# Kernel optimization log

Hardware: AMD Instinct MI355X
Metric: run time of the kernel (lower is better)

Reference implementation:

```python
import jax, jax.numpy as jnp
import numpy as np

N_NODES = 20000
N_EDGES = 200000
D_IN, D_H1, D_H2, D_OUT = 1433, 1000, 500, 7


def setup_inputs() -> dict:
    key = jax.random.key(0)
    ks = jax.random.split(key, 8)
    features = jax.random.normal(ks[0], (N_NODES, D_IN), dtype=jnp.float32)
    src = jax.random.randint(ks[1], (N_EDGES,), 0, N_NODES)
    dst = jax.random.randint(ks[2], (N_EDGES,), 0, N_NODES)
    W1 = jax.random.normal(ks[3], (D_IN, D_H1), dtype=jnp.float32) * 0.02
    b1 = jnp.zeros((D_H1,), dtype=jnp.float32)
    W2 = jax.random.normal(ks[4], (D_H1, D_H2), dtype=jnp.float32) * 0.02
    b2 = jnp.zeros((D_H2,), dtype=jnp.float32)
    W3 = jax.random.normal(ks[5], (D_H2, D_OUT), dtype=jnp.float32) * 0.02
    b3 = jnp.zeros((D_OUT,), dtype=jnp.float32)
    return {"features": features, "src": src, "dst": dst,
            "W1": W1, "b1": b1, "W2": W2, "b2": b2, "W3": W3, "b3": b3}


def reference(features, src, dst, W1, b1, W2, b2, W3, b3):
    N = features.shape[0]

    def agg(x):  # sum_tensors over incoming neighbors: h_i = sum_{(j->i) in E} x_j
        return jax.ops.segment_sum(x[src], dst, num_segments=N)

    # GCN layer 1: aggregate -> linear -> relu
    x = jax.nn.relu(agg(features) @ W1 + b1)       # [N, 1000]
    # GCN layer 2: aggregate -> linear -> relu (dropout = identity in eval)
    x = jax.nn.relu(agg(x) @ W2 + b2)              # [N, 500]
    # output linear -> relu (dropout = identity in eval)
    x = jax.nn.relu(x @ W3 + b3)                   # [N, 7]
    return x
```

## Files before the change

### kernel.cpp

```cpp
#include <hip/hip_runtime.h>
#include <hip/hip_bf16.h>


#define N_NODES 20000
#define N_EDGES 200000
#define D_IN    1433
#define D_H1    1000
#define D_H2    500
#define D_OUT   7

#define MPAD    20096
#define K1PAD   1472
#define N1PAD   1024
#define K2PAD   1024
#define N2PAD   512
#define MBLK    157
#define SCAN_N  (N_NODES + 1)
#define TB1     ((N1PAD / 32) * (K1PAD / 32))
#define TB2     ((N2PAD / 32) * (K2PAD / 32))
#define CNTB    ((N_EDGES + 255) / 256)

typedef __attribute__((ext_vector_type(8))) short short8;
typedef __attribute__((ext_vector_type(8))) unsigned short ushort8_t;
typedef __attribute__((ext_vector_type(4))) float f32x4;

__device__ __forceinline__ unsigned short bf16_rne(float x) {
    unsigned int u = __float_as_uint(x);
    u = (u + 0x7FFFu + ((u >> 16) & 1u)) >> 16;
    return (unsigned short)u;
}
__device__ __forceinline__ float bf16_up(unsigned short h) {
    return __uint_as_float((unsigned int)h << 16);
}

__device__ __forceinline__ void gl_lds16(const unsigned short* g, unsigned short* lds) {
    __builtin_amdgcn_global_load_lds(
        (const __attribute__((address_space(1))) unsigned int*)g,
        (__attribute__((address_space(3))) unsigned int*)lds, 16, 0, 0);
}

__global__ __launch_bounds__(256) void prep(const float* __restrict__ F,
                                            unsigned int* __restrict__ Fout,
                                            const float* __restrict__ W1,
                                            unsigned short* __restrict__ W1T,
                                            const float* __restrict__ W2,
                                            unsigned short* __restrict__ W2T,
                                            const int* __restrict__ dst,
                                            int* __restrict__ offs) {
    __shared__ float tile[32][33];
    const int bid = blockIdx.x, t = threadIdx.x;
    if (bid < MPAD) {
        int e = bid * 256 + t;
        if (e < N_EDGES) atomicAdd(&offs[dst[e] + 1], 1);
        const float* fr = F + (size_t)bid * D_IN;
        bool live = bid < N_NODES;
        for (int kk = t; kk < K1PAD / 2; kk += 256) {
            int k0 = kk * 2;
            float a = (live && k0     < D_IN) ? fr[k0]     : 0.f;
            float b = (live && k0 + 1 < D_IN) ? fr[k0 + 1] : 0.f;
            Fout[(size_t)bid * (K1PAD / 2) + kk] =
                (unsigned int)bf16_rne(a) | ((unsigned int)bf16_rne(b) << 16);
        }
        return;
    }
    const float* src; unsigned short* dstp;
    int SR, SC, DR, DC, bx, by;
    if (bid < MPAD + TB1) {
        int l = bid - MPAD;
        bx = l % (N1PAD / 32); by = l / (N1PAD / 32);
        src = W1; dstp = W1T; SR = D_IN; SC = D_H1; DR = N1PAD; DC = K1PAD;
    } else {
        int l = bid - MPAD - TB1;
        bx = l % (N2PAD / 32); by = l / (N2PAD / 32);
        src = W2; dstp = W2T; SR = D_H1; SC = D_H2; DR = N2PAD; DC = K2PAD;
    }
    const int c0 = bx * 32, r0 = by * 32;
    const int tx = t & 31, ty = t >> 5;
    #pragma unroll
    for (int p = 0; p < 4; ++p) {
        int r = r0 + ty + p * 8, c = c0 + tx;
        tile[ty + p * 8][tx] = (r < SR && c < SC) ? src[(size_t)r * SC + c] : 0.f;
    }
    __syncthreads();
    #pragma unroll
    for (int p = 0; p < 4; ++p) {
        int dr = c0 + ty + p * 8;
        int dc = r0 + tx;
        if (dr < DR && dc < DC) dstp[(size_t)dr * DC + dc] = bf16_rne(tile[tx][ty + p * 8]);
    }
}

__global__ __launch_bounds__(1024) void scan_csr(int* __restrict__ offs) {
    __shared__ int wsum[16];
    const int t = threadIdx.x, lane = t & 63, wv = t >> 6;
    const int base = t * 20;
    int v[20];
    int run = 0;
    #pragma unroll
    for (int k = 0; k < 20; ++k) {
        int i = base + k;
        int x = (i < SCAN_N) ? offs[i] : 0;
        run += x;
        v[k] = run;
    }
    const int tot = run;
    int w = tot;
    #pragma unroll
    for (int s = 1; s < 64; s <<= 1) {
        int u = __shfl_up(w, s, 64);
        if (lane >= s) w += u;
    }
    if (lane == 63) wsum[wv] = w;
    __syncthreads();
    int prefix = w - tot;
    for (int k = 0; k < wv; ++k) prefix += wsum[k];
    #pragma unroll
    for (int k = 0; k < 20; ++k) {
        int i = base + k;
        if (i < SCAN_N) offs[i] = prefix + v[k];
    }
}

__global__ __launch_bounds__(256) void fill_csr(const int* __restrict__ src,
                                                const int* __restrict__ dst,
                                                int* __restrict__ offs,
                                                int* __restrict__ srcs) {
    int e = blockIdx.x * 256 + threadIdx.x;
    if (e < N_EDGES) {
        int pos = atomicAdd(&offs[dst[e]], 1);
        srcs[pos] = src[e];
    }
}

template <int KPAD, int NB>
__global__ __launch_bounds__(256) void gemm_mfma(const unsigned short* __restrict__ A,
                                                 const unsigned short* __restrict__ B,
                                                 unsigned short* __restrict__ C,
                                                 int M, int OSTR) {
    __shared__ __align__(16) unsigned short sA[128 * 64];
    __shared__ __align__(16) unsigned short sB[128 * 64];
    const int bid = blockIdx.x;
    const int xcd = bid & 7;
    const int tt  = bid >> 3;
    const int nb  = tt % NB;
    const int mb  = (tt / NB) * 8 + xcd;
    if (mb >= MBLK) return;

    const int t = threadIdx.x;
    const int w = t >> 6, lane = t & 63;
    const int m0 = mb * 128, n0 = nb * 128;
    const int wm = (w >> 1) * 64, wn = (w & 1) * 64;

    const int srowo = lane >> 3;
    const int skc   = ((lane & 7) ^ srowo) * 8;
    const int mrow = lane & 15, quad = lane >> 4;

    const unsigned short* Aptr = A + (size_t)(m0 + srowo) * KPAD + skc;
    const unsigned short* Bptr = B + (size_t)(n0 + srowo) * KPAD + skc;

    f32x4 acc[4][4] = {};

    for (int k0 = 0; k0 < KPAD; k0 += 64) {
        #pragma unroll
        for (int c = 0; c < 4; ++c) {
            const int rbase = c * 32 + w * 8;
            gl_lds16(Aptr + (size_t)rbase * KPAD, &sA[rbase * 64]);
            gl_lds16(Bptr + (size_t)rbase * KPAD, &sB[rbase * 64]);
        }
        Aptr += 64; Bptr += 64;
        __syncthreads();

        #pragma unroll
        for (int s = 0; s < 2; ++s) {
            short8 af[4], bf[4];
            #pragma unroll
            for (int mt = 0; mt < 4; ++mt) {
                int r = wm + mt * 16 + mrow;
                af[mt] = *(const short8*)&sA[r * 64 + (((s * 4 + quad) ^ (mrow & 7)) * 8)];
            }
            #pragma unroll
            for (int nt = 0; nt < 4; ++nt) {
                int r = wn + nt * 16 + mrow;
                bf[nt] = *(const short8*)&sB[r * 64 + (((s * 4 + quad) ^ (mrow & 7)) * 8)];
            }
            #pragma unroll
            for (int mt = 0; mt < 4; ++mt)
                #pragma unroll
                for (int nt = 0; nt < 4; ++nt)
                    acc[mt][nt] = __builtin_amdgcn_mfma_f32_16x16x32_bf16(
                        af[mt], bf[nt], acc[mt][nt], 0, 0, 0);
        }
        __syncthreads();
    }

    #pragma unroll
    for (int mt = 0; mt < 4; ++mt) {
        int m = m0 + wm + mt * 16 + quad * 4;
        #pragma unroll
        for (int nt = 0; nt < 4; ++nt) {
            int n = n0 + wn + nt * 16 + mrow;
            if (n >= OSTR) continue;
            #pragma unroll
            for (int r = 0; r < 4; ++r)
                if (m + r < M) C[(size_t)(m + r) * OSTR + n] = bf16_rne(acc[mt][nt][r]);
        }
    }
}

__global__ __launch_bounds__(128) void agg1_bf16(const unsigned short* __restrict__ H,
                                                 const int* __restrict__ offs,
                                                 const int* __restrict__ srcs,
                                                 const float* __restrict__ bias,
                                                 unsigned short* __restrict__ X,
                                                 int hstr) {
    const int i = blockIdx.x, t = threadIdx.x;
    const bool active = t < 125;
    const int tc = active ? t : 124;
    ushort8_t o = (ushort8_t)0;
    if (i < N_NODES) {
        const int end = offs[i];
        const int beg = i ? offs[i - 1] : 0;
        const unsigned short* Hc = H + tc * 8;
        float s[8] = {};
        int e = beg;
        for (; e + 8 <= end; e += 8) {
            int j0 = srcs[e],     j1 = srcs[e + 1], j2 = srcs[e + 2], j3 = srcs[e + 3];
            int j4 = srcs[e + 4], j5 = srcs[e + 5], j6 = srcs[e + 6], j7 = srcs[e + 7];
            ushort8_t v0 = *(const ushort8_t*)(Hc + (size_t)j0 * hstr);
            ushort8_t v1 = *(const ushort8_t*)(Hc + (size_t)j1 * hstr);
            ushort8_t v2 = *(const ushort8_t*)(Hc + (size_t)j2 * hstr);
            ushort8_t v3 = *(const ushort8_t*)(Hc + (size_t)j3 * hstr);
            ushort8_t v4 = *(const ushort8_t*)(Hc + (size_t)j4 * hstr);
            ushort8_t v5 = *(const ushort8_t*)(Hc + (size_t)j5 * hstr);
            ushort8_t v6 = *(const ushort8_t*)(Hc + (size_t)j6 * hstr);
            ushort8_t v7 = *(const ushort8_t*)(Hc + (size_t)j7 * hstr);
            #pragma unroll
            for (int u = 0; u < 8; ++u) {
                float t0 = (bf16_up(v0[u]) + bf16_up(v1[u])) +
                           (bf16_up(v2[u]) + bf16_up(v3[u]));
                float t1 = (bf16_up(v4[u]) + bf16_up(v5[u])) +
                           (bf16_up(v6[u]) + bf16_up(v7[u]));
                s[u] += t0 + t1;
            }
        }
        for (; e + 4 <= end; e += 4) {
            int j0 = srcs[e], j1 = srcs[e + 1], j2 = srcs[e + 2], j3 = srcs[e + 3];
            ushort8_t v0 = *(const ushort8_t*)(Hc + (size_t)j0 * hstr);
            ushort8_t v1 = *(const ushort8_t*)(Hc + (size_t)j1 * hstr);
            ushort8_t v2 = *(const ushort8_t*)(Hc + (size_t)j2 * hstr);
            ushort8_t v3 = *(const ushort8_t*)(Hc + (size_t)j3 * hstr);
            #pragma unroll
            for (int u = 0; u < 8; ++u)
                s[u] += (bf16_up(v0[u]) + bf16_up(v1[u])) +
                        (bf16_up(v2[u]) + bf16_up(v3[u]));
        }
        for (; e < end; ++e) {
            ushort8_t v = *(const ushort8_t*)(Hc + (size_t)srcs[e] * hstr);
            #pragma unroll
            for (int u = 0; u < 8; ++u) s[u] += bf16_up(v[u]);
        }
        if (active) {
            #pragma unroll
            for (int u = 0; u < 8; ++u)
                o[u] = bf16_rne(fmaxf(s[u] + bias[t * 8 + u], 0.f));
        }
    }
    *(ushort8_t*)(X + (size_t)i * K2PAD + t * 8) = o;
}

__global__ __launch_bounds__(64) void agg2_out(const unsigned short* __restrict__ H,
                                               const int* __restrict__ offs,
                                               const int* __restrict__ srcs,
                                               const float* __restrict__ b2,
                                               const float* __restrict__ W3,
                                               const float* __restrict__ b3,
                                               float* __restrict__ out,
                                               int hstr) {
    const int i = blockIdx.x, t = threadIdx.x;
    const int tc = t < 63 ? t : 62;
    const int end = offs[i];
    const int beg = i ? offs[i - 1] : 0;
    const unsigned short* Hc = H + tc * 8;
    float s[8] = {};
    int e = beg;
    for (; e + 8 <= end; e += 8) {
        int j0 = srcs[e],     j1 = srcs[e + 1], j2 = srcs[e + 2], j3 = srcs[e + 3];
        int j4 = srcs[e + 4], j5 = srcs[e + 5], j6 = srcs[e + 6], j7 = srcs[e + 7];
        ushort8_t v0 = *(const ushort8_t*)(Hc + (size_t)j0 * hstr);
        ushort8_t v1 = *(const ushort8_t*)(Hc + (size_t)j1 * hstr);
        ushort8_t v2 = *(const ushort8_t*)(Hc + (size_t)j2 * hstr);
        ushort8_t v3 = *(const ushort8_t*)(Hc + (size_t)j3 * hstr);
        ushort8_t v4 = *(const ushort8_t*)(Hc + (size_t)j4 * hstr);
        ushort8_t v5 = *(const ushort8_t*)(Hc + (size_t)j5 * hstr);
        ushort8_t v6 = *(const ushort8_t*)(Hc + (size_t)j6 * hstr);
        ushort8_t v7 = *(const ushort8_t*)(Hc + (size_t)j7 * hstr);
        #pragma unroll
        for (int u = 0; u < 8; ++u) {
            float t0 = (bf16_up(v0[u]) + bf16_up(v1[u])) +
                       (bf16_up(v2[u]) + bf16_up(v3[u]));
            float t1 = (bf16_up(v4[u]) + bf16_up(v5[u])) +
                       (bf16_up(v6[u]) + bf16_up(v7[u]));
            s[u] += t0 + t1;
        }
    }
    for (; e + 4 <= end; e += 4) {
        int j0 = srcs[e], j1 = srcs[e + 1], j2 = srcs[e + 2], j3 = srcs[e + 3];
        ushort8_t v0 = *(const ushort8_t*)(Hc + (size_t)j0 * hstr);
        ushort8_t v1 = *(const ushort8_t*)(Hc + (size_t)j1 * hstr);
        ushort8_t v2 = *(const ushort8_t*)(Hc + (size_t)j2 * hstr);
        ushort8_t v3 = *(const ushort8_t*)(Hc + (size_t)j3 * hstr);
        #pragma unroll
        for (int u = 0; u < 8; ++u)
            s[u] += (bf16_up(v0[u]) + bf16_up(v1[u])) +
                    (bf16_up(v2[u]) + bf16_up(v3[u]));
    }
    for (; e < end; ++e) {
        ushort8_t v = *(const ushort8_t*)(Hc + (size_t)srcs[e] * hstr);
        #pragma unroll
        for (int u = 0; u < 8; ++u) s[u] += bf16_up(v[u]);
    }

    float acc[D_OUT] = {};
    if (t < 63) {
        #pragma unroll
        for (int u = 0; u < 8; ++u) {
            int col = t * 8 + u;
            if (col < D_H2) {
                float x = fmaxf(s[u] + b2[col], 0.f);
                const float* wr = W3 + (size_t)col * D_OUT;
                #pragma unroll
                for (int j = 0; j < D_OUT; ++j) acc[j] += x * wr[j];
            }
        }
    }
    #pragma unroll
    for (int j = 0; j < D_OUT; ++j)
        #pragma unroll
        for (int off = 32; off; off >>= 1) acc[j] += __shfl_down(acc[j], off);
    if (t == 0) {
        #pragma unroll
        for (int j = 0; j < D_OUT; ++j)
            out[(size_t)i * D_OUT + j] = fmaxf(acc[j] + b3[j], 0.f);
    }
}

extern "C" void kernel_launch(void* const* d_in, const int* in_sizes, int n_in,
                              void* d_out, int out_size, void* d_ws, size_t ws_size,
                              hipStream_t stream) {
    const float* features = (const float*)d_in[0];
    const int*   src      = (const int*)d_in[1];
    const int*   dst      = (const int*)d_in[2];
    const float* W1       = (const float*)d_in[3];
    const float* b1       = (const float*)d_in[4];
    const float* W2       = (const float*)d_in[5];
    const float* b2       = (const float*)d_in[6];
    const float* W3       = (const float*)d_in[7];
    const float* b3       = (const float*)d_in[8];
    float* out = (float*)d_out;

    const size_t FBF_B  = (size_t)MPAD * K1PAD * 2;
    const size_t W1T_B  = (size_t)N1PAD * K1PAD * 2;
    const size_t W2T_B  = (size_t)N2PAD * K2PAD * 2;
    const size_t OFFS_B = (size_t)SCAN_N * 4;
    const size_t bigNeed = FBF_B + (size_t)N_NODES * 1088 * 2 + W1T_B + W2T_B + OFFS_B;
    const bool big = ws_size >= bigNeed;
    const int h1str = big ? 1088 : 1008;
    const int h2str = big ? 576  : 504;

    char* ws = (char*)d_ws;
    unsigned short* Fbf  = (unsigned short*)(ws + 0);
    unsigned short* X1bf = (unsigned short*)(ws + 0);
    unsigned short* H1   = (unsigned short*)(ws + FBF_B);
    unsigned short* H2   = (unsigned short*)(ws + FBF_B);
    size_t oW1T = FBF_B + (size_t)N_NODES * h1str * 2;
    unsigned short* W1T  = (unsigned short*)(ws + oW1T);
    unsigned short* W2T  = (unsigned short*)(ws + oW1T + W1T_B);
    int* offs = (int*)(ws + oW1T + W1T_B + W2T_B);
    int* srcs = (int*)(ws + oW1T);

    hipMemsetAsync(offs, 0, SCAN_N * sizeof(int), stream);

    prep<<<MPAD + TB1 + TB2, 256, 0, stream>>>(
        features, (unsigned int*)Fbf, W1, W1T, W2, W2T, dst, offs);

    scan_csr<<<1, 1024, 0, stream>>>(offs);

    gemm_mfma<K1PAD, N1PAD / 128><<<8 * (N1PAD / 128) * 20, 256, 0, stream>>>(
        Fbf, W1T, H1, N_NODES, h1str);

    fill_csr<<<CNTB, 256, 0, stream>>>(src, dst, offs, srcs);

    agg1_bf16<<<MPAD, 128, 0, stream>>>(H1, offs, srcs, b1, X1bf, h1str);

    gemm_mfma<K2PAD, N2PAD / 128><<<8 * (N2PAD / 128) * 20, 256, 0, stream>>>(
        X1bf, W2T, H2, N_NODES, h2str);

    agg2_out<<<N_NODES, 64, 0, stream>>>(H2, offs, srcs, b2, W3, b3, out, h2str);
}
```

Before: 421.0 us.

## Split layer-1 aggregation into column chunks with edge-parallel lanes per node

Replaces the one-block-per-node aggregation with a kernel where each wave handles one node and one 64-column chunk. Eight lane groups each take a different edge, and their partial sums are combined with cross-lane shuffles. The chunk index is the slowest-varying part of the block id, so all nodes sweep the same column slice of H1 at roughly the same time. This is meant to improve cache locality of the random gathers and to expose more memory-level parallelism. In exchange, only one of eight lane groups does the final write, chunks past column 1000 do extra zero work, and every wave reads the CSR indices again for each chunk.

```diff
diff --git a/kernel.cpp b/kernel.cpp
--- a/kernel.cpp
+++ b/kernel.cpp
@@ -19,6 +19,8 @@
 #define TB1     ((N1PAD / 32) * (K1PAD / 32))
 #define TB2     ((N2PAD / 32) * (K2PAD / 32))
 #define CNTB    ((N_EDGES + 255) / 256)
+#define NCHUNK1 16
+#define NB4     (MPAD / 4)
 
 typedef __attribute__((ext_vector_type(8))) short short8;
 typedef __attribute__((ext_vector_type(8))) unsigned short ushort8_t;
@@ -207,65 +209,50 @@
     }
 }
 
-__global__ __launch_bounds__(128) void agg1_bf16(const unsigned short* __restrict__ H,
-                                                 const int* __restrict__ offs,
-                                                 const int* __restrict__ srcs,
-                                                 const float* __restrict__ bias,
-                                                 unsigned short* __restrict__ X,
-                                                 int hstr) {
-    const int i = blockIdx.x, t = threadIdx.x;
-    const bool active = t < 125;
-    const int tc = active ? t : 124;
+__global__ __launch_bounds__(256) void agg1_chunk(const unsigned short* __restrict__ H,
+                                                  const int* __restrict__ offs,
+                                                  const int* __restrict__ srcs,
+                                                  const float* __restrict__ bias,
+                                                  unsigned short* __restrict__ X,
+                                                  int hstr) {
+    const int bx = blockIdx.x;
+    const int c  = bx / NB4;
+    const int i  = (bx % NB4) * 4 + (threadIdx.x >> 6);
+    const int lane = threadIdx.x & 63;
+    const int g = lane >> 3, sub = lane & 7;
+    const int c0 = c * 64;
     ushort8_t o = (ushort8_t)0;
     if (i < N_NODES) {
         const int end = offs[i];
         const int beg = i ? offs[i - 1] : 0;
-        const unsigned short* Hc = H + tc * 8;
+        const unsigned short* Hc = H + c0 + sub * 8;
         float s[8] = {};
-        int e = beg;
-        for (; e + 8 <= end; e += 8) {
-            int j0 = srcs[e],     j1 = srcs[e + 1], j2 = srcs[e + 2], j3 = srcs[e + 3];
-            int j4 = srcs[e + 4], j5 = srcs[e + 5], j6 = srcs[e + 6], j7 = srcs[e + 7];
-            ushort8_t v0 = *(const ushort8_t*)(Hc + (size_t)j0 * hstr);
-            ushort8_t v1 = *(const ushort8_t*)(Hc + (size_t)j1 * hstr);
-            ushort8_t v2 = *(const ushort8_t*)(Hc + (size_t)j2 * hstr);
-            ushort8_t v3 = *(const ushort8_t*)(Hc + (size_t)j3 * hstr);
-            ushort8_t v4 = *(const ushort8_t*)(Hc + (size_t)j4 * hstr);
-            ushort8_t v5 = *(const ushort8_t*)(Hc + (size_t)j5 * hstr);
-            ushort8_t v6 = *(const ushort8_t*)(Hc + (size_t)j6 * hstr);
-            ushort8_t v7 = *(const ushort8_t*)(Hc + (size_t)j7 * hstr);
+        for (int e0 = beg; e0 < end; e0 += 8) {
+            int edge = e0 + g;
+            if (edge < end) {
+                int j = srcs[edge];
+                ushort8_t v = *(const ushort8_t*)(Hc + (size_t)j * hstr);
+                #pragma unroll
+                for (int u = 0; u < 8; ++u) s[u] += bf16_up(v[u]);
+            }
+        }
+        #pragma unroll
+        for (int u = 0; u < 8; ++u) {
+            s[u] += __shfl_xor(s[u], 8, 64);
+            s[u] += __shfl_xor(s[u], 16, 64);
+            s[u] += __shfl_xor(s[u], 32, 64);
+        }
+        if (g == 0) {
             #pragma unroll
             for (int u = 0; u < 8; ++u) {
-                float t0 = (bf16_up(v0[u]) + bf16_up(v1[u])) +
-                           (bf16_up(v2[u]) + bf16_up(v3[u]));
-                float t1 = (bf16_up(v4[u]) + bf16_up(v5[u])) +
-                           (bf16_up(v6[u]) + bf16_up(v7[u]));
-                s[u] += t0 + t1;
-            }
-        }
-        for (; e + 4 <= end; e += 4) {
-            int j0 = srcs[e], j1 = srcs[e + 1], j2 = srcs[e + 2], j3 = srcs[e + 3];
-            ushort8_t v0 = *(const ushort8_t*)(Hc + (size_t)j0 * hstr);
-            ushort8_t v1 = *(const ushort8_t*)(Hc + (size_t)j1 * hstr);
-            ushort8_t v2 = *(const ushort8_t*)(Hc + (size_t)j2 * hstr);
-            ushort8_t v3 = *(const ushort8_t*)(Hc + (size_t)j3 * hstr);
-            #pragma unroll
-            for (int u = 0; u < 8; ++u)
-                s[u] += (bf16_up(v0[u]) + bf16_up(v1[u])) +
-                        (bf16_up(v2[u]) + bf16_up(v3[u]));
-        }
-        for (; e < end; ++e) {
-            ushort8_t v = *(const ushort8_t*)(Hc + (size_t)srcs[e] * hstr);
-            #pragma unroll
-            for (int u = 0; u < 8; ++u) s[u] += bf16_up(v[u]);
-        }
-        if (active) {
-            #pragma unroll
-            for (int u = 0; u < 8; ++u)
-                o[u] = bf16_rne(fmaxf(s[u] + bias[t * 8 + u], 0.f));
-        }
-    }
-    *(ushort8_t*)(X + (size_t)i * K2PAD + t * 8) = o;
+                int col = c0 + sub * 8 + u;
+                float b = (col < D_H1) ? bias[col] : 0.f;
+                o[u] = bf16_rne(fmaxf(s[u] + b, 0.f));
+            }
+        }
+    }
+    if (g == 0)
+        *(ushort8_t*)(X + (size_t)i * K2PAD + c0 + sub * 8) = o;
 }
 
 __global__ __launch_bounds__(64) void agg2_out(const unsigned short* __restrict__ H,
@@ -390,7 +377,7 @@
 
     fill_csr<<<CNTB, 256, 0, stream>>>(src, dst, offs, srcs);
 
-    agg1_bf16<<<MPAD, 128, 0, stream>>>(H1, offs, srcs, b1, X1bf, h1str);
+    agg1_chunk<<<NCHUNK1 * NB4, 256, 0, stream>>>(H1, offs, srcs, b1, X1bf, h1str);
 
     gemm_mfma<K2PAD, N2PAD / 128><<<8 * (N2PAD / 128) * 20, 256, 0, stream>>>(
         X1bf, W2T, H2, N_NODES, h2str);
```

Result: slower. 489.2 us (+16.2%).
